# Optimization experiments

Measured on AMD Instinct MI355X. Metric: run time of the kernel, lower is better.

The kernel has to match this reference:

```python
import jax, jax.numpy as jnp
import numpy as np

B, C_IN, C_OUT, N, MODES = 16, 128, 128, 16384, 128

def setup_inputs() -> dict:
    key = jax.random.key(0)
    k1, k2, k3, k4 = jax.random.split(key, 4)
    scale = 1.0 / (C_IN * C_OUT)
    x = jax.random.normal(k1, (B, C_IN, N), dtype=jnp.float32)
    wbases = jax.random.normal(k2, (N, MODES), dtype=jnp.float32)
    bases = jax.random.normal(k3, (N, MODES), dtype=jnp.float32)
    W = scale * jax.random.uniform(k4, (C_IN, C_OUT, MODES), dtype=jnp.float32)
    return {"x": x, "wbases": wbases, "bases": bases, "W": W}

def reference(x, wbases, bases, W):
    # project onto weighted bases: [B, C_in, N] x [N, K] -> [B, C_in, K]
    x_co = jnp.einsum('bcx,xk->bck', x, wbases)
    # per-mode channel mixing: [B, C_in, K] x [C_in, C_out, K] -> [B, C_out, K]
    x_hat = jnp.einsum('bik,iok->bok', x_co, W)
    # reconstruct: [B, C_out, K] x [N, K] -> [B, C_out, N]
    return jnp.einsum('bok,xk->box', x_hat, bases)
```

## Files before the change

kernel.cpp:

```cpp
#include <hip/hip_runtime.h>
#include <hip/hip_bf16.h>
#include <stdint.h>

#define NB 16
#define NC 128
#define NK 128
#define NSP 16384
#define SPLIT 32
#define CHUNK 512
#define BK 64

typedef float f32x4 __attribute__((ext_vector_type(4)));
typedef __bf16 bf16x8 __attribute__((ext_vector_type(8)));

__device__ __forceinline__ unsigned short f32_to_bf16(float a) {
  unsigned int u = __float_as_uint(a);
  return (unsigned short)((u + 0x7fffu + ((u >> 16) & 1u)) >> 16);
}

__device__ __forceinline__ unsigned int pack_bf16(float a, float b) {
  unsigned int ua = __float_as_uint(a);
  unsigned int ub = __float_as_uint(b);
  ua = (ua + 0x7fffu + ((ua >> 16) & 1u)) >> 16;
  ub = (ub + 0x7fffu + ((ub >> 16) & 1u)) & 0xffff0000u;
  return ua | ub;
}

__device__ __forceinline__ void gl_lds16(const void* g, void* l) {
  __builtin_amdgcn_global_load_lds(
      (const __attribute__((address_space(1))) unsigned int*)g,
      (__attribute__((address_space(3))) unsigned int*)l, 16, 0, 0);
}

__global__ void k0_prep(const float* __restrict__ wb, unsigned short* __restrict__ wbT,
                        const float* __restrict__ bases, unsigned short* __restrict__ bb) {
  __shared__ float tile[32][33];
  if (blockIdx.x < 2048) {
    int bid = blockIdx.x;
    int kt = (bid & 3) * 32;
    int nt = (bid >> 2) * 32;
    int tx = threadIdx.x & 31;
    int ty = threadIdx.x >> 5;
#pragma unroll
    for (int i = 0; i < 32; i += 8)
      tile[ty + i][tx] = wb[(size_t)(nt + ty + i) * NK + kt + tx];
    __syncthreads();
#pragma unroll
    for (int i = 0; i < 32; i += 8)
      wbT[(size_t)(kt + ty + i) * NSP + nt + tx] = f32_to_bf16(tile[tx][ty + i]);
  } else {
    int i = (blockIdx.x - 2048) * 256 + threadIdx.x;
    float4 v = ((const float4*)bases)[i];
    uint2 o;
    o.x = pack_bf16(v.x, v.y);
    o.y = pack_bf16(v.z, v.w);
    ((uint2*)bb)[i] = o;
  }
}

__global__ __launch_bounds__(512, 4)
void k1_proj(const float* __restrict__ x, const unsigned short* __restrict__ wbT,
             float* __restrict__ part) {
  int blk = blockIdx.x;
  int b = blk >> 5;
  int chunk = blk & 31;
  int n0 = chunk * CHUNK;
  __shared__ unsigned short ldsA[2][8 * 128 * 8];
  __shared__ unsigned short ldsB[2][128 * 64];
  int tid = threadIdx.x;
  int lane = tid & 63;
  int wave = tid >> 6;
  int cb = (wave & 1) * 64;
  int kb = (wave >> 1) * 32;
  int r = lane & 15;
  int q = lane >> 4;

  f32x4 acc[4][2];
#pragma unroll
  for (int t = 0; t < 4; ++t)
#pragma unroll
    for (int u = 0; u < 2; ++u) acc[t][u] = (f32x4){0.f, 0.f, 0.f, 0.f};

  int g = tid & 7;
  int row0 = tid >> 3;
  const float* xbase = x + (size_t)(b * NC) * NSP + n0 + g * 8;

  const unsigned short* wsrc =
      wbT + n0 + (size_t)(lane >> 3) * NSP + ((lane & 7) ^ (lane >> 3)) * 8;

#pragma unroll
  for (int j = 0; j < 2; ++j) {
    int i = wave * 2 + j;
    gl_lds16(wsrc + (size_t)(i * 8) * NSP, (char*)ldsB[0] + i * 1024);
  }
  {
    uint4* wA = (uint4*)ldsA[0];
#pragma unroll
    for (int jj = 0; jj < 2; ++jj) {
      int row = row0 + jj * 64;
      const float4* p = (const float4*)(xbase + (size_t)row * NSP);
      float4 a0 = p[0];
      float4 a1 = p[1];
      uint4 u;
      u.x = pack_bf16(a0.x, a0.y);
      u.y = pack_bf16(a0.z, a0.w);
      u.z = pack_bf16(a1.x, a1.y);
      u.w = pack_bf16(a1.z, a1.w);
      wA[g * 128 + row] = u;
    }
  }
  __syncthreads();

  for (int it = 0; it < CHUNK / BK; ++it) {
    int cur = it & 1;
    bool pf = (it + 1) < (CHUNK / BK);
    float4 a0[2], a1[2];
    if (pf) {
#pragma unroll
      for (int j = 0; j < 2; ++j) {
        int i = wave * 2 + j;
        gl_lds16(wsrc + (size_t)(i * 8) * NSP + (it + 1) * BK,
                 (char*)ldsB[cur ^ 1] + i * 1024);
      }
#pragma unroll
      for (int jj = 0; jj < 2; ++jj) {
        int row = row0 + jj * 64;
        const float4* p = (const float4*)(xbase + (size_t)row * NSP + (it + 1) * BK);
        a0[jj] = p[0];
        a1[jj] = p[1];
      }
    }
    const bf16x8* pA = (const bf16x8*)ldsA[cur];
    const char* pB = (const char*)ldsB[cur];
#pragma unroll
    for (int s = 0; s < 2; ++s) {
      bf16x8 af[4], bf[2];
      int s4q = s * 4 + q;
#pragma unroll
      for (int t = 0; t < 4; ++t) af[t] = pA[s4q * 128 + cb + 16 * t + r];
#pragma unroll
      for (int u = 0; u < 2; ++u) {
        int rw = kb + 16 * u + r;
        bf[u] = *(const bf16x8*)(pB + rw * 128 + ((s4q ^ (r & 7)) << 4));
      }
#pragma unroll
      for (int t = 0; t < 4; ++t)
#pragma unroll
        for (int u = 0; u < 2; ++u)
          acc[t][u] = __builtin_amdgcn_mfma_f32_16x16x32_bf16(af[t], bf[u],
                                                              acc[t][u], 0, 0, 0);
    }
    if (pf) {
      uint4* wA = (uint4*)ldsA[cur ^ 1];
#pragma unroll
      for (int jj = 0; jj < 2; ++jj) {
        int row = row0 + jj * 64;
        uint4 u;
        u.x = pack_bf16(a0[jj].x, a0[jj].y);
        u.y = pack_bf16(a0[jj].z, a0[jj].w);
        u.z = pack_bf16(a1[jj].x, a1[jj].y);
        u.w = pack_bf16(a1[jj].z, a1[jj].w);
        wA[g * 128 + row] = u;
      }
    }
    __syncthreads();
  }

  float* pp = part + (size_t)blk * (NC * NK);
  int rq = q * 4;
#pragma unroll
  for (int t = 0; t < 4; ++t)
#pragma unroll
    for (int u = 0; u < 2; ++u)
#pragma unroll
      for (int v = 0; v < 4; ++v)
        pp[(cb + 16 * t + rq + v) * NK + kb + 16 * u + r] = acc[t][u][v];
}

__global__ __launch_bounds__(256)
void k1b_reduce(const float* __restrict__ part, float* __restrict__ x_co) {
  int idx = blockIdx.x * 256 + threadIdx.x;
  int b = idx >> 13;
  int r2 = idx & 8191;
  const float2* p = (const float2*)(part + (size_t)b * SPLIT * (NC * NK)) + r2;
  float2 s = {0.f, 0.f};
#pragma unroll
  for (int c = 0; c < SPLIT; ++c) {
    float2 v = p[(size_t)c * (NC * NK / 2)];
    s.x += v.x;
    s.y += v.y;
  }
  ((float2*)x_co)[idx] = s;
}

__global__ __launch_bounds__(128)
void k2_mix(const float* __restrict__ x_co, const float* __restrict__ W,
            unsigned short* __restrict__ xhat_bf) {
  int b = blockIdx.x >> 6;
  int o0 = (blockIdx.x & 63) * 2;
  int k = threadIdx.x;
  const float* xc = x_co + (size_t)b * NC * NK + k;
  const float* w0 = W + (size_t)o0 * NK + k;
  float a0 = 0.f, a1 = 0.f;
#pragma unroll 4
  for (int i = 0; i < NC; ++i) {
    float v = xc[(size_t)i * NK];
    a0 += v * w0[(size_t)i * (NC * NK)];
    a1 += v * w0[(size_t)i * (NC * NK) + NK];
  }
  size_t base = ((size_t)b * NC + o0) * NK + k;
  xhat_bf[base] = f32_to_bf16(a0);
  xhat_bf[base + NK] = f32_to_bf16(a1);
}

__global__ __launch_bounds__(256, 2)
void k3_recon(const unsigned short* __restrict__ xhat_bf,
              const unsigned short* __restrict__ bases_bf,
              float* __restrict__ out) {
  int blk = blockIdx.x;
  int mo0 = (blk & 15) * 128;
  int n0 = (blk >> 4) * 512;
  __shared__ unsigned short ldsB[2][128 * 128];
  int tid = threadIdx.x;
  int lane = tid & 63;
  int wave = tid >> 6;
  int mb = (wave & 1) * 64;
  int nb = (wave >> 1) * 64;
  int r = lane & 15;
  int q = lane >> 4;

  bf16x8 af[4][4];
#pragma unroll
  for (int t = 0; t < 4; ++t)
#pragma unroll
    for (int s = 0; s < 4; ++s)
      af[t][s] = *(const bf16x8*)(xhat_bf +
                                  (size_t)(mo0 + mb + 16 * t + r) * NK +
                                  s * 32 + q * 8);

  int rlane = lane >> 4;
  int slane = lane & 15;

#pragma unroll
  for (int jj = 0; jj < 8; ++jj) {
    int i = wave * 8 + jj;
    int c = slane ^ (((i & 3) << 2) | rlane);
    gl_lds16(bases_bf + (size_t)(n0 + i * 4 + rlane) * NK + c * 8,
             (char*)ldsB[0] + i * 1024);
  }

  for (int sub = 0; sub < 4; ++sub) {
    __syncthreads();
    int cur = sub & 1;
    if (sub < 3) {
#pragma unroll
      for (int jj = 0; jj < 8; ++jj) {
        int i = wave * 8 + jj;
        int c = slane ^ (((i & 3) << 2) | rlane);
        gl_lds16(bases_bf + (size_t)(n0 + (sub + 1) * 128 + i * 4 + rlane) * NK + c * 8,
                 (char*)ldsB[cur ^ 1] + i * 1024);
      }
    }
    const char* bbuf = (const char*)ldsB[cur];
    f32x4 acc[4][4];
#pragma unroll
    for (int t = 0; t < 4; ++t)
#pragma unroll
      for (int u = 0; u < 4; ++u) acc[t][u] = (f32x4){0.f, 0.f, 0.f, 0.f};
#pragma unroll
    for (int s = 0; s < 4; ++s) {
      bf16x8 bf[4];
      int s4q = s * 4 + q;
#pragma unroll
      for (int u = 0; u < 4; ++u) {
        int rw = nb + 16 * u + r;
        bf[u] = *(const bf16x8*)(bbuf + rw * 256 + ((s4q ^ r) << 4));
      }
#pragma unroll
      for (int t = 0; t < 4; ++t)
#pragma unroll
        for (int u = 0; u < 4; ++u)
          acc[t][u] = __builtin_amdgcn_mfma_f32_16x16x32_bf16(af[t][s], bf[u],
                                                              acc[t][u], 0, 0, 0);
    }
    int rq = q * 4;
#pragma unroll
    for (int t = 0; t < 4; ++t)
#pragma unroll
      for (int u = 0; u < 4; ++u)
#pragma unroll
        for (int v = 0; v < 4; ++v)
          out[(size_t)(mo0 + mb + 16 * t + rq + v) * NSP + n0 + sub * 128 +
              nb + 16 * u + r] = acc[t][u][v];
  }
}

extern "C" void kernel_launch(void* const* d_in, const int* in_sizes, int n_in,
                              void* d_out, int out_size, void* d_ws, size_t ws_size,
                              hipStream_t stream) {
  const float* x = (const float*)d_in[0];
  const float* wbases = (const float*)d_in[1];
  const float* bases = (const float*)d_in[2];
  const float* W = (const float*)d_in[3];
  float* out = (float*)d_out;

  char* ws = (char*)d_ws;
  if (ws_size < ((size_t)42 << 20)) return;
  unsigned short* wbT = (unsigned short*)(ws);
  unsigned short* bases_bf = (unsigned short*)(ws + ((size_t)4 << 20));
  float* part = (float*)(ws + ((size_t)8 << 20));
  float* x_co = (float*)(ws + ((size_t)40 << 20));
  unsigned short* xhat_bf = (unsigned short*)(ws + ((size_t)41 << 20));

  k0_prep<<<4096, 256, 0, stream>>>(wbases, wbT, bases, bases_bf);
  k1_proj<<<NB * SPLIT, 512, 0, stream>>>(x, wbT, part);
  k1b_reduce<<<512, 256, 0, stream>>>(part, x_co);
  k2_mix<<<NB * NC / 2, 128, 0, stream>>>(x_co, W, xhat_bf);
  k3_recon<<<512, 256, 0, stream>>>(xhat_bf, bases_bf, out);
}
```

Measured before the change: 300.2 us.

## Fuse prep, projection, reduce and mix into one cooperative kernel with grid syncs

Replaces four separate launches (weight transpose/convert, projection GEMM, split reduction, channel mixing) with a single cooperative kernel of 512 blocks that separates the phases with grid.sync(). The goal is to remove launch gaps and tail effects between the small phases. In exchange the prep and mix phases are remapped onto the fixed grid, which may lower their parallelism, and the grid-wide barriers add their own cost. A fallback to the old multi-kernel path remains in case the cooperative launch fails, and the fallback k2_mix now computes one output per block.

```diff
diff --git a/kernel.cpp b/kernel.cpp
--- a/kernel.cpp
+++ b/kernel.cpp
@@ -1,6 +1,9 @@
 #include <hip/hip_runtime.h>
 #include <hip/hip_bf16.h>
+#include <hip/hip_cooperative_groups.h>
 #include <stdint.h>
+
+namespace cg = cooperative_groups;
 
 #define NB 16
 #define NC 128
@@ -30,6 +33,188 @@
   __builtin_amdgcn_global_load_lds(
       (const __attribute__((address_space(1))) unsigned int*)g,
       (__attribute__((address_space(3))) unsigned int*)l, 16, 0, 0);
+}
+
+__global__ __launch_bounds__(512, 4)
+void mega(const float* __restrict__ x, const float* __restrict__ wb,
+          const float* __restrict__ bases, const float* __restrict__ W,
+          unsigned short* __restrict__ wbT, unsigned short* __restrict__ bases_bf,
+          float* __restrict__ part, float* __restrict__ x_co,
+          unsigned short* __restrict__ xhat_bf) {
+  cg::grid_group grid = cg::this_grid();
+  __shared__ __align__(16) char raw[65536];
+  int blk = blockIdx.x;
+  int tid = threadIdx.x;
+  int gt = blk * 512 + tid;
+
+  {
+    float(*tile)[32][33] = (float(*)[32][33])raw;
+    int h = tid >> 8;
+    int vt = tid & 255;
+    int tx = vt & 31, ty = vt >> 5;
+#pragma unroll
+    for (int rep = 0; rep < 2; ++rep) {
+      int vb = blk * 2 + h + rep * 1024;
+      int kt = (vb & 3) * 32, nt = (vb >> 2) * 32;
+#pragma unroll
+      for (int i = 0; i < 32; i += 8)
+        tile[h][ty + i][tx] = wb[(size_t)(nt + ty + i) * NK + kt + tx];
+      __syncthreads();
+#pragma unroll
+      for (int i = 0; i < 32; i += 8)
+        wbT[(size_t)(kt + ty + i) * NSP + nt + tx] =
+            f32_to_bf16(tile[h][tx][ty + i]);
+      __syncthreads();
+    }
+#pragma unroll
+    for (int rep = 0; rep < 2; ++rep) {
+      int i = gt + rep * 262144;
+      float4 v = ((const float4*)bases)[i];
+      uint2 o;
+      o.x = pack_bf16(v.x, v.y);
+      o.y = pack_bf16(v.z, v.w);
+      ((uint2*)bases_bf)[i] = o;
+    }
+  }
+  grid.sync();
+
+  {
+    int b = blk >> 5;
+    int chunk = blk & 31;
+    int n0 = chunk * CHUNK;
+    int lane = tid & 63;
+    int wave = tid >> 6;
+    int cb = (wave & 1) * 64;
+    int kb = (wave >> 1) * 32;
+    int r = lane & 15;
+    int q = lane >> 4;
+
+    f32x4 acc[4][2];
+#pragma unroll
+    for (int t = 0; t < 4; ++t)
+#pragma unroll
+      for (int u = 0; u < 2; ++u) acc[t][u] = (f32x4){0.f, 0.f, 0.f, 0.f};
+
+    int g = tid & 7;
+    int row0 = tid >> 3;
+    const float* xbase = x + (size_t)(b * NC) * NSP + n0 + g * 8;
+    const unsigned short* wsrc =
+        wbT + n0 + (size_t)(lane >> 3) * NSP + ((lane & 7) ^ (lane >> 3)) * 8;
+
+#pragma unroll
+    for (int j = 0; j < 2; ++j) {
+      int i = wave * 2 + j;
+      gl_lds16(wsrc + (size_t)(i * 8) * NSP, raw + 32768 + i * 1024);
+    }
+    {
+      uint4* wA = (uint4*)raw;
+#pragma unroll
+      for (int jj = 0; jj < 2; ++jj) {
+        int row = row0 + jj * 64;
+        const float4* p = (const float4*)(xbase + (size_t)row * NSP);
+        float4 a0 = p[0];
+        float4 a1 = p[1];
+        uint4 u;
+        u.x = pack_bf16(a0.x, a0.y);
+        u.y = pack_bf16(a0.z, a0.w);
+        u.z = pack_bf16(a1.x, a1.y);
+        u.w = pack_bf16(a1.z, a1.w);
+        wA[g * 128 + row] = u;
+      }
+    }
+    __syncthreads();
+
+    for (int it = 0; it < CHUNK / BK; ++it) {
+      int cur = it & 1;
+      bool pf = (it + 1) < (CHUNK / BK);
+      float4 a0[2], a1[2];
+      if (pf) {
+#pragma unroll
+        for (int j = 0; j < 2; ++j) {
+          int i = wave * 2 + j;
+          gl_lds16(wsrc + (size_t)(i * 8) * NSP + (it + 1) * BK,
+                   raw + 32768 + (cur ^ 1) * 16384 + i * 1024);
+        }
+#pragma unroll
+        for (int jj = 0; jj < 2; ++jj) {
+          int row = row0 + jj * 64;
+          const float4* p =
+              (const float4*)(xbase + (size_t)row * NSP + (it + 1) * BK);
+          a0[jj] = p[0];
+          a1[jj] = p[1];
+        }
+      }
+      const bf16x8* pA = (const bf16x8*)(raw + cur * 16384);
+      const char* pB = raw + 32768 + cur * 16384;
+#pragma unroll
+      for (int s = 0; s < 2; ++s) {
+        bf16x8 af[4], bf[2];
+        int s4q = s * 4 + q;
+#pragma unroll
+        for (int t = 0; t < 4; ++t) af[t] = pA[s4q * 128 + cb + 16 * t + r];
+#pragma unroll
+        for (int u = 0; u < 2; ++u) {
+          int rw = kb + 16 * u + r;
+          bf[u] = *(const bf16x8*)(pB + rw * 128 + ((s4q ^ (r & 7)) << 4));
+        }
+#pragma unroll
+        for (int t = 0; t < 4; ++t)
+#pragma unroll
+          for (int u = 0; u < 2; ++u)
+            acc[t][u] = __builtin_amdgcn_mfma_f32_16x16x32_bf16(
+                af[t], bf[u], acc[t][u], 0, 0, 0);
+      }
+      if (pf) {
+        uint4* wA = (uint4*)(raw + (cur ^ 1) * 16384);
+#pragma unroll
+        for (int jj = 0; jj < 2; ++jj) {
+          int row = row0 + jj * 64;
+          uint4 u;
+          u.x = pack_bf16(a0[jj].x, a0[jj].y);
+          u.y = pack_bf16(a0[jj].z, a0[jj].w);
+          u.z = pack_bf16(a1[jj].x, a1[jj].y);
+          u.w = pack_bf16(a1[jj].z, a1[jj].w);
+          wA[g * 128 + row] = u;
+        }
+      }
+      __syncthreads();
+    }
+
+    float* pp = part + (size_t)blk * (NC * NK);
+    int rq = q * 4;
+#pragma unroll
+    for (int t = 0; t < 4; ++t)
+#pragma unroll
+      for (int u = 0; u < 2; ++u)
+#pragma unroll
+        for (int v = 0; v < 4; ++v)
+          pp[(cb + 16 * t + rq + v) * NK + kb + 16 * u + r] = acc[t][u][v];
+  }
+  grid.sync();
+
+  {
+    int b = gt >> 14;
+    int rk = gt & 16383;
+    const float* p = part + (size_t)b * SPLIT * (NC * NK) + rk;
+    float s = 0.f;
+#pragma unroll
+    for (int c = 0; c < SPLIT; ++c) s += p[(size_t)c * (NC * NK)];
+    x_co[gt] = s;
+  }
+  grid.sync();
+
+  {
+    int b = gt >> 14;
+    int o = (gt >> 7) & 127;
+    int k = gt & 127;
+    const float* xc = x_co + (size_t)b * NC * NK + k;
+    const float* wp = W + (size_t)o * NK + k;
+    float acc = 0.f;
+#pragma unroll 4
+    for (int i = 0; i < NC; ++i)
+      acc += xc[(size_t)i * NK] * wp[(size_t)i * (NC * NK)];
+    xhat_bf[gt] = f32_to_bf16(acc);
+  }
 }
 
 __global__ void k0_prep(const float* __restrict__ wb, unsigned short* __restrict__ wbT,
@@ -74,20 +259,16 @@
   int kb = (wave >> 1) * 32;
   int r = lane & 15;
   int q = lane >> 4;
-
   f32x4 acc[4][2];
 #pragma unroll
   for (int t = 0; t < 4; ++t)
 #pragma unroll
     for (int u = 0; u < 2; ++u) acc[t][u] = (f32x4){0.f, 0.f, 0.f, 0.f};
-
   int g = tid & 7;
   int row0 = tid >> 3;
   const float* xbase = x + (size_t)(b * NC) * NSP + n0 + g * 8;
-
   const unsigned short* wsrc =
       wbT + n0 + (size_t)(lane >> 3) * NSP + ((lane & 7) ^ (lane >> 3)) * 8;
-
 #pragma unroll
   for (int j = 0; j < 2; ++j) {
     int i = wave * 2 + j;
@@ -110,7 +291,6 @@
     }
   }
   __syncthreads();
-
   for (int it = 0; it < CHUNK / BK; ++it) {
     int cur = it & 1;
     bool pf = (it + 1) < (CHUNK / BK);
@@ -165,7 +345,6 @@
     }
     __syncthreads();
   }
-
   float* pp = part + (size_t)blk * (NC * NK);
   int rq = q * 4;
 #pragma unroll
@@ -196,21 +375,16 @@
 __global__ __launch_bounds__(128)
 void k2_mix(const float* __restrict__ x_co, const float* __restrict__ W,
             unsigned short* __restrict__ xhat_bf) {
-  int b = blockIdx.x >> 6;
-  int o0 = (blockIdx.x & 63) * 2;
+  int b = blockIdx.x >> 7;
+  int o = blockIdx.x & 127;
   int k = threadIdx.x;
   const float* xc = x_co + (size_t)b * NC * NK + k;
-  const float* w0 = W + (size_t)o0 * NK + k;
-  float a0 = 0.f, a1 = 0.f;
+  const float* wp = W + (size_t)o * NK + k;
+  float acc = 0.f;
 #pragma unroll 4
-  for (int i = 0; i < NC; ++i) {
-    float v = xc[(size_t)i * NK];
-    a0 += v * w0[(size_t)i * (NC * NK)];
-    a1 += v * w0[(size_t)i * (NC * NK) + NK];
-  }
-  size_t base = ((size_t)b * NC + o0) * NK + k;
-  xhat_bf[base] = f32_to_bf16(a0);
-  xhat_bf[base + NK] = f32_to_bf16(a1);
+  for (int i = 0; i < NC; ++i)
+    acc += xc[(size_t)i * NK] * wp[(size_t)i * (NC * NK)];
+  xhat_bf[((size_t)b * NC + o) * NK + k] = f32_to_bf16(acc);
 }
 
 __global__ __launch_bounds__(256, 2)
@@ -312,9 +486,16 @@
   float* x_co = (float*)(ws + ((size_t)40 << 20));
   unsigned short* xhat_bf = (unsigned short*)(ws + ((size_t)41 << 20));
 
-  k0_prep<<<4096, 256, 0, stream>>>(wbases, wbT, bases, bases_bf);
-  k1_proj<<<NB * SPLIT, 512, 0, stream>>>(x, wbT, part);
-  k1b_reduce<<<512, 256, 0, stream>>>(part, x_co);
-  k2_mix<<<NB * NC / 2, 128, 0, stream>>>(x_co, W, xhat_bf);
+  void* args[] = {(void*)&x, (void*)&wbases, (void*)&bases, (void*)&W,
+                  (void*)&wbT, (void*)&bases_bf, (void*)&part,
+                  (void*)&x_co, (void*)&xhat_bf};
+  hipError_t err = hipLaunchCooperativeKernel((const void*)mega, dim3(512),
+                                              dim3(512), args, 0, stream);
+  if (err != hipSuccess) {
+    k0_prep<<<4096, 256, 0, stream>>>(wbases, wbT, bases, bases_bf);
+    k1_proj<<<NB * SPLIT, 512, 0, stream>>>(x, wbT, part);
+    k1b_reduce<<<512, 256, 0, stream>>>(part, x_co);
+    k2_mix<<<NB * NC, 128, 0, stream>>>(x_co, W, xhat_bf);
+  }
   k3_recon<<<512, 256, 0, stream>>>(xhat_bf, bases_bf, out);
 }
```

Measured after the change: 487.9 us. 1.62x slower.

## Drop LDS staging in projection and reconstruction, load MFMA fragments from global

Applied to the files above, without the earlier changes.

Both GEMM kernels stop staging tiles through LDS with double-buffered async loads and instead load MFMA operand fragments straight from global memory into registers. The projection kernel is split into two K halves with 256-thread blocks and twice as many blocks, and the reconstruction kernel halves its N range per block, doubling the grid and occupancy. This removes LDS traffic and barrier stalls but relies on L1/L2 for reuse, and the x rows are now read and converted to bf16 twice, once per K half, with less coalesced row-strided loads.

```diff
diff --git a/kernel.cpp b/kernel.cpp
--- a/kernel.cpp
+++ b/kernel.cpp
@@ -26,10 +26,13 @@
   return ua | ub;
 }
 
-__device__ __forceinline__ void gl_lds16(const void* g, void* l) {
-  __builtin_amdgcn_global_load_lds(
-      (const __attribute__((address_space(1))) unsigned int*)g,
-      (__attribute__((address_space(3))) unsigned int*)l, 16, 0, 0);
+__device__ __forceinline__ bf16x8 pack8(float4 a0, float4 a1) {
+  uint4 u;
+  u.x = pack_bf16(a0.x, a0.y);
+  u.y = pack_bf16(a0.z, a0.w);
+  u.z = pack_bf16(a1.x, a1.y);
+  u.w = pack_bf16(a1.z, a1.w);
+  return __builtin_bit_cast(bf16x8, u);
 }
 
 __global__ void k0_prep(const float* __restrict__ wb, unsigned short* __restrict__ wbT,
@@ -58,20 +61,19 @@
   }
 }
 
-__global__ __launch_bounds__(512, 4)
+__global__ __launch_bounds__(256, 4)
 void k1_proj(const float* __restrict__ x, const unsigned short* __restrict__ wbT,
              float* __restrict__ part) {
   int blk = blockIdx.x;
-  int b = blk >> 5;
+  int khalf = blk >> 9;
+  int b = (blk >> 5) & 15;
   int chunk = blk & 31;
   int n0 = chunk * CHUNK;
-  __shared__ unsigned short ldsA[2][8 * 128 * 8];
-  __shared__ unsigned short ldsB[2][128 * 64];
   int tid = threadIdx.x;
   int lane = tid & 63;
   int wave = tid >> 6;
   int cb = (wave & 1) * 64;
-  int kb = (wave >> 1) * 32;
+  int kb = khalf * 64 + (wave >> 1) * 32;
   int r = lane & 15;
   int q = lane >> 4;
 
@@ -81,68 +83,23 @@
 #pragma unroll
     for (int u = 0; u < 2; ++u) acc[t][u] = (f32x4){0.f, 0.f, 0.f, 0.f};
 
-  int g = tid & 7;
-  int row0 = tid >> 3;
-  const float* xbase = x + (size_t)(b * NC) * NSP + n0 + g * 8;
-
-  const unsigned short* wsrc =
-      wbT + n0 + (size_t)(lane >> 3) * NSP + ((lane & 7) ^ (lane >> 3)) * 8;
-
-#pragma unroll
-  for (int j = 0; j < 2; ++j) {
-    int i = wave * 2 + j;
-    gl_lds16(wsrc + (size_t)(i * 8) * NSP, (char*)ldsB[0] + i * 1024);
-  }
-  {
-    uint4* wA = (uint4*)ldsA[0];
-#pragma unroll
-    for (int jj = 0; jj < 2; ++jj) {
-      int row = row0 + jj * 64;
-      const float4* p = (const float4*)(xbase + (size_t)row * NSP);
-      float4 a0 = p[0];
-      float4 a1 = p[1];
-      uint4 u;
-      u.x = pack_bf16(a0.x, a0.y);
-      u.y = pack_bf16(a0.z, a0.w);
-      u.z = pack_bf16(a1.x, a1.y);
-      u.w = pack_bf16(a1.z, a1.w);
-      wA[g * 128 + row] = u;
-    }
-  }
-  __syncthreads();
-
+  const float* xrow = x + (size_t)(b * NC + cb + r) * NSP + n0;
+  const unsigned short* wrow = wbT + (size_t)(kb + r) * NSP + n0;
+
+#pragma unroll 2
   for (int it = 0; it < CHUNK / BK; ++it) {
-    int cur = it & 1;
-    bool pf = (it + 1) < (CHUNK / BK);
-    float4 a0[2], a1[2];
-    if (pf) {
-#pragma unroll
-      for (int j = 0; j < 2; ++j) {
-        int i = wave * 2 + j;
-        gl_lds16(wsrc + (size_t)(i * 8) * NSP + (it + 1) * BK,
-                 (char*)ldsB[cur ^ 1] + i * 1024);
+#pragma unroll
+    for (int s = 0; s < 2; ++s) {
+      int c2 = it * BK + s * 32 + q * 8;
+      bf16x8 af[4], bf[2];
+#pragma unroll
+      for (int t = 0; t < 4; ++t) {
+        const float4* p = (const float4*)(xrow + (size_t)t * 16 * NSP + c2);
+        af[t] = pack8(p[0], p[1]);
       }
 #pragma unroll
-      for (int jj = 0; jj < 2; ++jj) {
-        int row = row0 + jj * 64;
-        const float4* p = (const float4*)(xbase + (size_t)row * NSP + (it + 1) * BK);
-        a0[jj] = p[0];
-        a1[jj] = p[1];
-      }
-    }
-    const bf16x8* pA = (const bf16x8*)ldsA[cur];
-    const char* pB = (const char*)ldsB[cur];
-#pragma unroll
-    for (int s = 0; s < 2; ++s) {
-      bf16x8 af[4], bf[2];
-      int s4q = s * 4 + q;
-#pragma unroll
-      for (int t = 0; t < 4; ++t) af[t] = pA[s4q * 128 + cb + 16 * t + r];
-#pragma unroll
-      for (int u = 0; u < 2; ++u) {
-        int rw = kb + 16 * u + r;
-        bf[u] = *(const bf16x8*)(pB + rw * 128 + ((s4q ^ (r & 7)) << 4));
-      }
+      for (int u = 0; u < 2; ++u)
+        bf[u] = *(const bf16x8*)(wrow + (size_t)u * 16 * NSP + c2);
 #pragma unroll
       for (int t = 0; t < 4; ++t)
 #pragma unroll
@@ -150,23 +107,9 @@
           acc[t][u] = __builtin_amdgcn_mfma_f32_16x16x32_bf16(af[t], bf[u],
                                                               acc[t][u], 0, 0, 0);
     }
-    if (pf) {
-      uint4* wA = (uint4*)ldsA[cur ^ 1];
-#pragma unroll
-      for (int jj = 0; jj < 2; ++jj) {
-        int row = row0 + jj * 64;
-        uint4 u;
-        u.x = pack_bf16(a0[jj].x, a0[jj].y);
-        u.y = pack_bf16(a0[jj].z, a0[jj].w);
-        u.z = pack_bf16(a1[jj].x, a1[jj].y);
-        u.w = pack_bf16(a1[jj].z, a1[jj].w);
-        wA[g * 128 + row] = u;
-      }
-    }
-    __syncthreads();
-  }
-
-  float* pp = part + (size_t)blk * (NC * NK);
+  }
+
+  float* pp = part + (size_t)(b * SPLIT + chunk) * (NC * NK);
   int rq = q * 4;
 #pragma unroll
   for (int t = 0; t < 4; ++t)
@@ -213,14 +156,13 @@
   xhat_bf[base + NK] = f32_to_bf16(a1);
 }
 
-__global__ __launch_bounds__(256, 2)
+__global__ __launch_bounds__(256, 4)
 void k3_recon(const unsigned short* __restrict__ xhat_bf,
               const unsigned short* __restrict__ bases_bf,
               float* __restrict__ out) {
   int blk = blockIdx.x;
   int mo0 = (blk & 15) * 128;
-  int n0 = (blk >> 4) * 512;
-  __shared__ unsigned short ldsB[2][128 * 128];
+  int n0 = (blk >> 4) * 256;
   int tid = threadIdx.x;
   int lane = tid & 63;
   int wave = tid >> 6;
@@ -228,40 +170,14 @@
   int nb = (wave >> 1) * 64;
   int r = lane & 15;
   int q = lane >> 4;
-
-  bf16x8 af[4][4];
-#pragma unroll
-  for (int t = 0; t < 4; ++t)
-#pragma unroll
-    for (int s = 0; s < 4; ++s)
-      af[t][s] = *(const bf16x8*)(xhat_bf +
-                                  (size_t)(mo0 + mb + 16 * t + r) * NK +
-                                  s * 32 + q * 8);
-
-  int rlane = lane >> 4;
-  int slane = lane & 15;
-
-#pragma unroll
-  for (int jj = 0; jj < 8; ++jj) {
-    int i = wave * 8 + jj;
-    int c = slane ^ (((i & 3) << 2) | rlane);
-    gl_lds16(bases_bf + (size_t)(n0 + i * 4 + rlane) * NK + c * 8,
-             (char*)ldsB[0] + i * 1024);
-  }
-
-  for (int sub = 0; sub < 4; ++sub) {
-    __syncthreads();
-    int cur = sub & 1;
-    if (sub < 3) {
-#pragma unroll
-      for (int jj = 0; jj < 8; ++jj) {
-        int i = wave * 8 + jj;
-        int c = slane ^ (((i & 3) << 2) | rlane);
-        gl_lds16(bases_bf + (size_t)(n0 + (sub + 1) * 128 + i * 4 + rlane) * NK + c * 8,
-                 (char*)ldsB[cur ^ 1] + i * 1024);
-      }
-    }
-    const char* bbuf = (const char*)ldsB[cur];
+  int rq = q * 4;
+
+  const unsigned short* arow = xhat_bf + (size_t)(mo0 + mb + r) * NK + q * 8;
+
+#pragma unroll
+  for (int sub = 0; sub < 2; ++sub) {
+    const unsigned short* brow =
+        bases_bf + (size_t)(n0 + sub * 128 + nb + r) * NK + q * 8;
     f32x4 acc[4][4];
 #pragma unroll
     for (int t = 0; t < 4; ++t)
@@ -269,29 +185,28 @@
       for (int u = 0; u < 4; ++u) acc[t][u] = (f32x4){0.f, 0.f, 0.f, 0.f};
 #pragma unroll
     for (int s = 0; s < 4; ++s) {
-      bf16x8 bf[4];
-      int s4q = s * 4 + q;
-#pragma unroll
-      for (int u = 0; u < 4; ++u) {
-        int rw = nb + 16 * u + r;
-        bf[u] = *(const bf16x8*)(bbuf + rw * 256 + ((s4q ^ r) << 4));
-      }
+      bf16x8 af[4], bf[4];
 #pragma unroll
       for (int t = 0; t < 4; ++t)
+        af[t] = *(const bf16x8*)(arow + (size_t)t * 16 * NK + s * 32);
+#pragma unroll
+      for (int u = 0; u < 4; ++u)
+        bf[u] = *(const bf16x8*)(brow + (size_t)u * 16 * NK + s * 32);
+#pragma unroll
+      for (int t = 0; t < 4; ++t)
 #pragma unroll
         for (int u = 0; u < 4; ++u)
-          acc[t][u] = __builtin_amdgcn_mfma_f32_16x16x32_bf16(af[t][s], bf[u],
+          acc[t][u] = __builtin_amdgcn_mfma_f32_16x16x32_bf16(af[t], bf[u],
                                                               acc[t][u], 0, 0, 0);
     }
-    int rq = q * 4;
+    float* obase = out + (size_t)(mo0 + mb + rq) * NSP + n0 + sub * 128 + nb + r;
 #pragma unroll
     for (int t = 0; t < 4; ++t)
 #pragma unroll
       for (int u = 0; u < 4; ++u)
 #pragma unroll
         for (int v = 0; v < 4; ++v)
-          out[(size_t)(mo0 + mb + 16 * t + rq + v) * NSP + n0 + sub * 128 +
-              nb + 16 * u + r] = acc[t][u][v];
+          obase[(size_t)(16 * t + v) * NSP + 16 * u] = acc[t][u][v];
   }
 }
 
@@ -313,8 +228,8 @@
   unsigned short* xhat_bf = (unsigned short*)(ws + ((size_t)41 << 20));
 
   k0_prep<<<4096, 256, 0, stream>>>(wbases, wbT, bases, bases_bf);
-  k1_proj<<<NB * SPLIT, 512, 0, stream>>>(x, wbT, part);
+  k1_proj<<<1024, 256, 0, stream>>>(x, wbT, part);
   k1b_reduce<<<512, 256, 0, stream>>>(part, x_co);
   k2_mix<<<NB * NC / 2, 128, 0, stream>>>(x_co, W, xhat_bf);
-  k3_recon<<<512, 256, 0, stream>>>(xhat_bf, bases_bf, out);
-}
+  k3_recon<<<1024, 256, 0, stream>>>(xhat_bf, bases_bf, out);
+}
```

Result: slower. 360.7 us (+20.1%).
